# Performance work log

Hardware: AMD Instinct MI355X
Metric: run time of the kernel (lower is better)

Reference implementation:

```python
import jax, jax.numpy as jnp
import numpy as np

GAMMA = 0.999      # EMA momentum
M_PROTO = 10       # prototypes per class
K_CLS = 201        # 200 classes + background
EPS_SK = 0.05      # sinkhorn temperature
SK_ITERS = 3       # sinkhorn iterations
THR = 0.5          # pseudo-gt threshold
D_BB = 768         # backbone dim
D = 512            # projected dim


def _ln(x, g, b, eps=1e-5):
    mu = x.mean(-1, keepdims=True)
    var = ((x - mu) ** 2).mean(-1, keepdims=True)
    return (x - mu) / jnp.sqrt(var + eps) * g + b


def _l2n(x, eps=1e-12):
    n = jnp.linalg.norm(x, axis=-1, keepdims=True)
    return x / jnp.maximum(n, eps)


def _pca_dir(A, niter=10):
    # rank-1 PCA direction (deterministic power iteration; mirrors torch.pca_lowrank(q=1, center=True))
    Ac = A - A.mean(0, keepdims=True)
    v = jnp.ones((A.shape[1],), A.dtype) / jnp.sqrt(jnp.asarray(A.shape[1], A.dtype))
    for _ in range(niter):
        v = Ac.T @ (Ac @ v)
        v = v / jnp.linalg.norm(v)
    u = Ac @ v
    return u / jnp.linalg.norm(u)


def setup_inputs() -> dict:
    key = jax.random.key(0)
    ks = jax.random.split(key, 6)
    B, HW = 16, 1024
    return dict(
        patch_tokens=jax.random.normal(ks[0], (B, HW, D_BB), jnp.float32),
        gt=jax.random.randint(ks[1], (B,), 0, K_CLS - 1),
        proj_w=jax.random.normal(ks[2], (D, D_BB), jnp.float32) * 0.02,
        proj_b=jnp.zeros((D,), jnp.float32),
        feat_g=jnp.ones((D,), jnp.float32),
        feat_b=jnp.zeros((D,), jnp.float32),
        mask_g=jnp.ones((K_CLS,), jnp.float32),
        mask_b=jnp.zeros((K_CLS,), jnp.float32),
        prototypes=jax.random.normal(ks[3], (K_CLS, M_PROTO, D), jnp.float32) * 0.02,
    )


def reference(patch_tokens, gt, proj_w, proj_b, feat_g, feat_b, mask_g, mask_b, prototypes):
    B, HW, _ = patch_tokens.shape
    H = W = int(np.sqrt(HW))
    N = B * HW

    # ----- ged_pseudo_gt (on detached tokens) -----
    U = _pca_dir(patch_tokens.reshape(-1, D_BB))            # [N]
    Us = (U - U.min()) / (U.max() - U.min())
    Us = Us.reshape(B, H, W)
    pseudo_gt = jnp.where(Us < THR, gt[:, None, None], K_CLS - 1)  # [B,H,W]

    # ----- projection + normalization -----
    f = patch_tokens @ proj_w.T + proj_b                    # [B,HW,D]
    _c = _l2n(_ln(f.reshape(N, D), feat_g, feat_b))         # [N,D]
    protos = _l2n(prototypes)                               # buffer is l2-normalized in-place
    masks = jnp.einsum('nd,kmd->nmk', _c, protos)           # [N,M,K] cosine sims
    out_flat = _ln(masks.max(axis=1), mask_g, mask_b)       # [N,K]
    out_seg = out_flat.reshape(B, H, W, K_CLS).transpose(0, 3, 1, 2)  # [B,K,H,W]

    # ----- prototype_learning (vectorized 201-class loop) -----
    gt_seg = pseudo_gt.reshape(-1)                          # [N] int
    pred = jnp.argmax(out_flat, axis=-1)
    correct = (gt_seg == pred).astype(_c.dtype)             # [N]
    proto_logits = _c @ protos.reshape(-1, D).T             # [N, K*M]

    sel = jax.nn.one_hot(gt_seg, K_CLS, dtype=_c.dtype)     # [N,K] class membership
    Bk = sel.sum(0)                                         # pixels per class
    Bk_safe = jnp.where(Bk > 0, Bk, 1.0)

    # masked per-class sinkhorn (all classes in parallel)
    Q = jnp.exp(masks / EPS_SK) * sel[:, None, :]           # [N,M,K]
    sQ = Q.sum((0, 1))                                      # [K]
    Q = Q / jnp.where(sQ > 0, sQ, 1.0)
    for _ in range(SK_ITERS):
        row = Q.sum(0, keepdims=True)                       # [1,M,K] sum over pixels
        Q = Q / jnp.where(row > 0, row, 1.0) / M_PROTO
        col = Q.sum(1, keepdims=True)                       # [N,1,K] sum over prototypes
        Q = Q / jnp.where(col > 0, col, 1.0) / Bk_safe
    Q = Q * Bk                                              # [N,M,K]

    Qn = jnp.take_along_axis(Q, gt_seg[:, None, None], axis=2)[:, :, 0]  # [N,M]
    idx = jnp.argmax(Qn, axis=1)                            # hard assignment per pixel
    proto_target = (idx + M_PROTO * gt_seg).astype(jnp.float32)

    # EMA update: q masked by prediction correctness (m_k applies to both m_q and c_q; m_k^2 = m_k)
    q = jax.nn.one_hot(idx, M_PROTO, dtype=_c.dtype) * correct[:, None]  # [N,M]
    fproto = jnp.einsum('nk,nm,nd->kmd', sel, q, _c)        # per-(class,proto) feature sums
    ncnt = jnp.einsum('nk,nm->km', sel, q)                  # assignment counts
    fnorm = _l2n(fproto)
    upd = (ncnt != 0)[:, :, None]
    new_protos = _l2n(jnp.where(upd, GAMMA * protos + (1.0 - GAMMA) * fnorm, protos))

    return out_seg, proto_logits, proto_target, pseudo_gt, new_protos
```

## Files before the change

kernel.cpp:

```cpp
#include <hip/hip_runtime.h>
#include <cstdint>
#include <cstddef>

typedef _Float16 half8  __attribute__((ext_vector_type(8)));
typedef _Float16 half4v __attribute__((ext_vector_type(4)));
typedef float    f32x4  __attribute__((ext_vector_type(4)));

static constexpr int HWPX = 1024;
static constexpr int NPX  = 16384;
static constexpr int DBB  = 768;
static constexpr int DD   = 512;
static constexpr int KC   = 201;
static constexpr int KM   = 2010;
static constexpr int KMP  = 2048;

static constexpr size_t OFF_XCH    = 0;
static constexpr size_t OFF_TP     = 491520;
static constexpr size_t OFF_COLP   = 492160;
static constexpr size_t OFF_ROW16  = 541312;
static constexpr size_t OFF_ROW3   = 670336;
static constexpr size_t OFF_ROW5   = 678400;
static constexpr size_t OFF_BK     = 686464;
static constexpr size_t OFF_NCNT   = 687488;
static constexpr size_t OFF_FPROTO = 695552;
static constexpr size_t ZTOTAL     = 4812032;
static constexpr size_t OFF_GTSEG  = 4812032;
static constexpr size_t OFF_CORR   = 4877568;
static constexpr size_t OFF_U      = 4943104;
static constexpr size_t OFF_PN     = 5074176;
static constexpr size_t OFF_P16    = 9190656;
static constexpr size_t OFF_C16    = 11287808;
static constexpr size_t OFF_QD     = 28065024;
static constexpr size_t OFF_W16    = 28720384;

static constexpr size_t OUT_SEG = 0;
static constexpr size_t OUT_PL  = 3293184;
static constexpr size_t OUT_PT  = 36225024;
static constexpr size_t OUT_PG  = 36241408;
static constexpr size_t OUT_NP  = 36257792;

#define GLDS16(gp, lp) __builtin_amdgcn_global_load_lds( \
    (__attribute__((address_space(1))) const void*)(gp), \
    (__attribute__((address_space(3))) void*)(lp), 16, 0, 0)

static __device__ __forceinline__ float  wredf(float x){
  #pragma unroll
  for (int o=32;o;o>>=1) x += __shfl_down(x,o);
  return x;
}
static __device__ __forceinline__ double wredd(double x){
  #pragma unroll
  for (int o=32;o;o>>=1) x += __shfl_down(x,o);
  return x;
}

template<bool FIRST>
__global__ __launch_bounds__(256) void kPIter2(const float* __restrict__ A,
    const double* __restrict__ Win, const double* __restrict__ Tin, const double* __restrict__ colp,
    double* __restrict__ Wout, double* __restrict__ Tout, double* __restrict__ colout){
  __shared__ double vs[768];
  __shared__ double red[4][12][64];
  __shared__ double sT[4];
  int tid=threadIdx.x, lane=tid&63, w=tid>>6;
  if (FIRST){
    for (int cc=tid; cc<768; cc+=256) vs[cc] = 1.0/sqrt(768.0);
  } else {
    double Ts=0.0;
    #pragma unroll
    for (int p=0;p<8;p++) Ts += Tin[p];
    for (int cc=tid; cc<768; cc+=256){
      double sw=0.0, mc=0.0;
      #pragma unroll
      for (int p=0;p<8;p++){ sw += Win[p*768+cc]; mc += colp[p*768+cc]; }
      vs[cc] = sw - mc*(1.0/16384.0)*Ts;
    }
  }
  __syncthreads();
  int rbase = blockIdx.x*16 + w*4;
  double acc[12], cacc[12]; double tloc=0.0;
  #pragma unroll
  for (int j=0;j<12;j++){ acc[j]=0.0; cacc[j]=0.0; }
  for (int i=0;i<4;i++){
    const float* Ar = A + (size_t)(rbase+i)*DBB;
    double a[12]; double wp=0.0;
    #pragma unroll
    for (int j=0;j<12;j++){ int c=j*64+lane; a[j]=(double)Ar[c]; wp += a[j]*vs[c]; }
    wp = wredd(wp); wp = __shfl(wp,0);
    #pragma unroll
    for (int j=0;j<12;j++) acc[j] += wp*a[j];
    if (FIRST){
      #pragma unroll
      for (int j=0;j<12;j++) cacc[j] += a[j];
    }
    tloc += wp;
  }
  #pragma unroll
  for (int j=0;j<12;j++) red[w][j][lane]=acc[j];
  if (lane==0) sT[w]=tloc;
  __syncthreads();
  double* dst = Wout + (size_t)(blockIdx.x&7)*768;
  for (int cc=tid; cc<768; cc+=256){
    int j=cc>>6, l=cc&63;
    atomicAdd(&dst[cc], red[0][j][l]+red[1][j][l]+red[2][j][l]+red[3][j][l]);
  }
  if (tid==0) atomicAdd(&Tout[blockIdx.x&7], sT[0]+sT[1]+sT[2]+sT[3]);
  if (FIRST){
    __syncthreads();
    #pragma unroll
    for (int j=0;j<12;j++) red[w][j][lane]=cacc[j];
    __syncthreads();
    double* cdst = colout + (size_t)(blockIdx.x&7)*768;
    for (int cc=tid; cc<768; cc+=256){
      int j=cc>>6, l=cc&63;
      atomicAdd(&cdst[cc], red[0][j][l]+red[1][j][l]+red[2][j][l]+red[3][j][l]);
    }
  }
}

__global__ __launch_bounds__(256) void kPU2(const float* __restrict__ A, const double* __restrict__ Wp,
    const double* __restrict__ Tp, const double* __restrict__ colp, double* __restrict__ u){
  __shared__ double vs[768];
  __shared__ double sS[4];
  int tid=threadIdx.x, lane=tid&63, w=tid>>6;
  double Ts=0.0;
  #pragma unroll
  for (int p=0;p<8;p++) Ts += Tp[p];
  double sloc=0.0;
  for (int cc=tid; cc<768; cc+=256){
    double sw=0.0, mc=0.0;
    #pragma unroll
    for (int p=0;p<8;p++){ sw += Wp[p*768+cc]; mc += colp[p*768+cc]; }
    double m = mc*(1.0/16384.0);
    double v = sw - m*Ts;
    vs[cc] = v;
    sloc += m*v;
  }
  sloc = wredd(sloc);
  if (lane==0) sS[w]=sloc;
  __syncthreads();
  double s = sS[0]+sS[1]+sS[2]+sS[3];
  int rbase = blockIdx.x*16 + w*4;
  for (int i=0;i<4;i++){
    const float* Ar = A + (size_t)(rbase+i)*DBB;
    double wp=0.0;
    #pragma unroll
    for (int j=0;j<12;j++){ int c=j*64+lane; wp += (double)Ar[c]*vs[c]; }
    wp = wredd(wp);
    if (lane==0) u[rbase+i] = wp - s;
  }
}

__global__ __launch_bounds__(1024) void kFin(const double* __restrict__ u, const int* __restrict__ gt,
      float* __restrict__ outPG, int* __restrict__ gtseg, int* __restrict__ Bk){
  __shared__ double smn[16], smx[16];
  __shared__ double sres[2];
  int t = threadIdx.x;
  double mn=1e300, mx=-1e300;
  for (int k=0;k<16;k++){ double x=u[k*1024+t]; mn=fmin(mn,x); mx=fmax(mx,x); }
  #pragma unroll
  for (int o=32;o;o>>=1){ mn=fmin(mn,__shfl_down(mn,o)); mx=fmax(mx,__shfl_down(mx,o)); }
  if ((t&63)==0){ smn[t>>6]=mn; smx[t>>6]=mx; }
  __syncthreads();
  if (t==0){
    for (int i=1;i<16;i++){ mn=fmin(mn,smn[i]); mx=fmax(mx,smx[i]); }
    sres[0]=mn; sres[1]=mx;
  }
  __syncthreads();
  mn=sres[0]; mx=sres[1];
  double inv = 1.0/(mx-mn);
  for (int k=0;k<16;k++){
    int n = k*1024 + t;
    int c0 = gt[k];
    double us = (u[n]-mn)*inv;
    int g = (us < 0.5) ? c0 : 200;
    outPG[n] = (float)g;
    gtseg[n] = g;
    unsigned long long b0 = __ballot(g==c0);
    unsigned long long b1 = __ballot(g==200);
    if ((t&63)==0){
      atomicAdd(&Bk[c0], (int)__popcll(b0));
      atomicAdd(&Bk[200], (int)__popcll(b1));
    }
  }
}

__global__ __launch_bounds__(256) void kPrep(const float* __restrict__ Wp, _Float16* __restrict__ W16,
    const float* __restrict__ PR, float* __restrict__ Pn, _Float16* __restrict__ P16){
  int b = blockIdx.x;
  if (b < 384){
    int i = b*256 + threadIdx.x;
    float4 vv = ((const float4*)Wp)[i];
    half4v h; h[0]=(_Float16)vv.x; h[1]=(_Float16)vv.y; h[2]=(_Float16)vv.z; h[3]=(_Float16)vv.w;
    ((half4v*)W16)[i] = h;
    return;
  }
  int w=threadIdx.x>>6, lane=threadIdx.x&63;
  int km = (b-384)*4 + w;
  if (km >= KM){
    if (km < KMP){
      half8 z;
      #pragma unroll
      for (int i=0;i<8;i++) z[i]=(_Float16)0.0f;
      *(half8*)(P16 + (size_t)km*DD + lane*8) = z;
    }
    return;
  }
  const float* r = PR + (size_t)km*DD + lane*8;
  float4 a = *(const float4*)r, b2 = *(const float4*)(r+4);
  float x[8] = {a.x,a.y,a.z,a.w,b2.x,b2.y,b2.z,b2.w};
  float ss=0;
  #pragma unroll
  for (int i=0;i<8;i++) ss += x[i]*x[i];
  ss = __shfl(wredf(ss),0);
  float nrm = fmaxf(sqrtf(ss), 1e-12f);
  float* pw = Pn + (size_t)km*DD + lane*8;
  half8 h;
  #pragma unroll
  for (int i=0;i<8;i++){ float vv = x[i]/nrm; pw[i]=vv; h[i]=(_Float16)vv; }
  *(half8*)(P16 + (size_t)km*DD + lane*8) = h;
}

__global__ __launch_bounds__(256) void gemm1(const float* __restrict__ Af, const _Float16* __restrict__ Bm,
    _Float16* __restrict__ Ch, const float* __restrict__ bias){
  __shared__ __align__(16) char As[128*128];
  __shared__ __align__(16) char Bs[128*128];
  const int tid = threadIdx.x;
  const int lane = tid & 63, w = tid >> 6;
  const int wr = w >> 1, wc = w & 1;
  const int lrow = lane & 15, kg = lane >> 4;
  const int id = blockIdx.x;
  const int xcd = id & 7, pos = id >> 3;
  const int m0 = ((xcd<<4) | (pos>>2)) * 128;
  const int n0 = (pos & 3) * 128;

  f32x4 acc[4][4];
  #pragma unroll
  for (int i=0;i<4;i++)
    #pragma unroll
    for (int j=0;j<4;j++){ f32x4 z = {0.f,0.f,0.f,0.f}; acc[i][j]=z; }

  for (int k0 = 0; k0 < DBB; k0 += 64){
    #pragma unroll
    for (int i=0;i<4;i++){
      int slot = (i*4 + w)*64 + lane;
      int r = slot >> 3, c = slot & 7;
      int cs = c ^ (r & 7);
      GLDS16(Bm + (size_t)(n0+r)*DBB + k0 + cs*8, Bs + (i*4+w)*1024);
    }
    #pragma unroll
    for (int i=0;i<8;i++){
      int slot = i*256 + tid;
      int r = slot >> 4, c4 = slot & 15;
      float4 v = *(const float4*)(Af + (size_t)(m0+r)*DBB + k0 + c4*4);
      half4v h; h[0]=(_Float16)v.x; h[1]=(_Float16)v.y; h[2]=(_Float16)v.z; h[3]=(_Float16)v.w;
      *(half4v*)(As + r*128 + (((c4>>1)^(r&7))<<4) + (c4&1)*8) = h;
    }
    __syncthreads();
    #pragma unroll
    for (int h=0; h<2; h++){
      half8 af[4], bf[4];
      #pragma unroll
      for (int mi=0;mi<4;mi++){
        int ar = wr*64 + mi*16 + lrow;
        af[mi] = *(const half8*)(As + ar*128 + (((h*4+kg) ^ (ar&7))<<4));
      }
      #pragma unroll
      for (int nj=0;nj<4;nj++){
        int br = wc*64 + nj*16 + lrow;
        bf[nj] = *(const half8*)(Bs + br*128 + (((h*4+kg) ^ (br&7))<<4));
      }
      #pragma unroll
      for (int mi=0;mi<4;mi++)
        #pragma unroll
        for (int nj=0;nj<4;nj++)
          acc[mi][nj] = __builtin_amdgcn_mfma_f32_16x16x32_f16(af[mi], bf[nj], acc[mi][nj], 0,0,0);
    }
    __syncthreads();
  }
  #pragma unroll
  for (int mi=0;mi<4;mi++){
    int gr = m0 + wr*64 + mi*16 + kg*4;
    #pragma unroll
    for (int nj=0;nj<4;nj++){
      int gc = n0 + wc*64 + nj*16 + lrow;
      float bv = bias[gc];
      #pragma unroll
      for (int r2=0;r2<4;r2++)
        Ch[(size_t)(gr+r2)*DD + gc] = (_Float16)(acc[mi][nj][r2] + bv);
    }
  }
}

__global__ __launch_bounds__(256) void gemm2(const _Float16* __restrict__ Am, const _Float16* __restrict__ Bm,
    float* __restrict__ Cf){
  __shared__ __align__(16) char As[128*128];
  __shared__ __align__(16) char Bs[128*128];
  const int tid = threadIdx.x;
  const int lane = tid & 63, w = tid >> 6;
  const int wr = w >> 1, wc = w & 1;
  const int lrow = lane & 15, kg = lane >> 4;
  const int id = blockIdx.x;
  const int xcd = id & 7, pos = id >> 3;
  const int m0 = ((xcd<<4) | (pos>>4)) * 128;
  const int n0 = (pos & 15) * 128;

  f32x4 acc[4][4];
  #pragma unroll
  for (int i=0;i<4;i++)
    #pragma unroll
    for (int j=0;j<4;j++){ f32x4 z = {0.f,0.f,0.f,0.f}; acc[i][j]=z; }

  for (int k0 = 0; k0 < DD; k0 += 64){
    #pragma unroll
    for (int i=0;i<4;i++){
      int slot = (i*4 + w)*64 + lane;
      int r = slot >> 3, c = slot & 7;
      int cs = c ^ (r & 7);
      GLDS16(Am + (size_t)(m0+r)*DD + k0 + cs*8, As + (i*4+w)*1024);
      GLDS16(Bm + (size_t)(n0+r)*DD + k0 + cs*8, Bs + (i*4+w)*1024);
    }
    __syncthreads();
    #pragma unroll
    for (int h=0; h<2; h++){
      half8 af[4], bf[4];
      #pragma unroll
      for (int mi=0;mi<4;mi++){
        int ar = wr*64 + mi*16 + lrow;
        af[mi] = *(const half8*)(As + ar*128 + (((h*4+kg) ^ (ar&7))<<4));
      }
      #pragma unroll
      for (int nj=0;nj<4;nj++){
        int br = wc*64 + nj*16 + lrow;
        bf[nj] = *(const half8*)(Bs + br*128 + (((h*4+kg) ^ (br&7))<<4));
      }
      #pragma unroll
      for (int mi=0;mi<4;mi++)
        #pragma unroll
        for (int nj=0;nj<4;nj++)
          acc[mi][nj] = __builtin_amdgcn_mfma_f32_16x16x32_f16(af[mi], bf[nj], acc[mi][nj], 0,0,0);
    }
    __syncthreads();
  }
  #pragma unroll
  for (int mi=0;mi<4;mi++){
    int gr = m0 + wr*64 + mi*16 + kg*4;
    #pragma unroll
    for (int nj=0;nj<4;nj++){
      int gc = n0 + wc*64 + nj*16 + lrow;
      if (gc < KM){
        #pragma unroll
        for (int r2=0;r2<4;r2++)
          Cf[(size_t)(gr+r2)*KM + gc] = acc[mi][nj][r2];
      }
    }
  }
}

__global__ __launch_bounds__(256) void kLNl2n(_Float16* __restrict__ C16,
      const float* __restrict__ fg, const float* __restrict__ fb){
  int w=threadIdx.x>>6, lane=threadIdx.x&63;
  int n = blockIdx.x*4 + w;
  _Float16* row = C16 + (size_t)n*DD + lane*8;
  half8 h = *(const half8*)row;
  float x[8];
  #pragma unroll
  for (int i=0;i<8;i++) x[i] = (float)h[i];
  float s=0;
  #pragma unroll
  for (int i=0;i<8;i++) s += x[i];
  float mu = __shfl(wredf(s),0)/512.f;
  float q=0;
  #pragma unroll
  for (int i=0;i<8;i++){ float d=x[i]-mu; q+=d*d; }
  float var = __shfl(wredf(q),0)/512.f;
  float inv = 1.f/sqrtf(var+1e-5f);
  float4 g0 = *(const float4*)(fg+lane*8), g1 = *(const float4*)(fg+lane*8+4);
  float4 b0 = *(const float4*)(fb+lane*8), b1 = *(const float4*)(fb+lane*8+4);
  float gg[8] = {g0.x,g0.y,g0.z,g0.w,g1.x,g1.y,g1.z,g1.w};
  float bb[8] = {b0.x,b0.y,b0.z,b0.w,b1.x,b1.y,b1.z,b1.w};
  float y[8]; float ss=0;
  #pragma unroll
  for (int i=0;i<8;i++){ y[i] = (x[i]-mu)*inv*gg[i]+bb[i]; ss += y[i]*y[i]; }
  float nrm = fmaxf(sqrtf(__shfl(wredf(ss),0)), 1e-12f);
  half8 o;
  #pragma unroll
  for (int i=0;i<8;i++) o[i] = (_Float16)(y[i]/nrm);
  *(half8*)row = o;
}

__global__ __launch_bounds__(256) void kMaxSK(const float* __restrict__ PL, const float* __restrict__ mg,
    const float* __restrict__ mb, const int* __restrict__ gtseg, const int* __restrict__ gt,
    float* __restrict__ outseg, int* __restrict__ corr, float* __restrict__ Qd, float* __restrict__ row16){
  __shared__ float tile[16][205];
  __shared__ float qpart[10][2];
  int tid=threadIdx.x, lane=tid&63, w=tid>>6;
  int n0 = blockIdx.x*16;
  int b = n0>>10, hw0 = n0&1023;
  int c0 = gt[b];
  if (tid<20) qpart[tid>>1][tid&1]=0.f;
  __syncthreads();
  for (int r=0;r<16;r++){
    int n = n0 + r;
    int g = gtseg[n];
    if (tid < KC){
      const float* src = PL + (size_t)n*KM + tid*10;
      float v[10];
      #pragma unroll
      for (int m2=0;m2<5;m2++){
        float2 t2 = *(const float2*)(src + m2*2);
        v[m2*2]=t2.x; v[m2*2+1]=t2.y;
      }
      float mx = v[0];
      #pragma unroll
      for (int m=1;m<10;m++) mx = fmaxf(mx,v[m]);
      tile[r][tid] = mx;
      if (tid == g){
        int cl = (g==200)?1:0;
        #pragma unroll
        for (int m=0;m<10;m++){
          float e = expf(v[m]*20.f);
          Qd[(size_t)n*10+m] = e;
          atomicAdd(&qpart[m][cl], e);
        }
      }
    }
  }
  __syncthreads();
  for (int rr=0; rr<4; ++rr){
    int r = w*4 + rr;
    int n = n0 + r;
    float xv[4]; int ncl=0;
    for (int c=lane;c<KC;c+=64) xv[ncl++] = tile[r][c];
    float ps=0;
    for (int i=0;i<ncl;i++) ps += xv[i];
    float mu = __shfl(wredf(ps),0)*(1.f/201.f);
    float pv=0;
    for (int i=0;i<ncl;i++){ float d=xv[i]-mu; pv+=d*d; }
    float var = __shfl(wredf(pv),0)*(1.f/201.f);
    float inv = 1.f/sqrtf(var+1e-5f);
    float bv=-3.0e38f; int bi=1<<30;
    ncl=0;
    for (int c=lane;c<KC;c+=64){
      float o = (xv[ncl]-mu)*inv*mg[c]+mb[c]; ncl++;
      tile[r][c] = o;
      if (o>bv){ bv=o; bi=c; }
    }
    #pragma unroll
    for (int o2=32;o2;o2>>=1){
      float ov=__shfl_down(bv,o2); int oi=__shfl_down(bi,o2);
      if (ov>bv||(ov==bv&&oi<bi)){bv=ov;bi=oi;}
    }
    if (lane==0) corr[n] = (bi==gtseg[n])?1:0;
  }
  __syncthreads();
  if (tid<20){
    int m=tid>>1, cl=tid&1;
    atomicAdd(&row16[(size_t)(blockIdx.x&15)*2016 + m*KC + (cl?200:c0)], qpart[m][cl]);
  }
  for (int idx=tid; idx<KC*16; idx+=256){
    int c=idx>>4, j=idx&15;
    outseg[(((size_t)b*KC+c)<<10) + hw0 + j] = tile[j][c];
  }
}

__global__ __launch_bounds__(256) void kSKpass(float* __restrict__ Qd, const int* __restrict__ gtseg,
      const int* __restrict__ gt, const float* __restrict__ rin, int rin_parts,
      float* __restrict__ rout, const int* __restrict__ Bk){
  __shared__ float rin2[10][2];
  __shared__ double part[4][10][2];
  int n = blockIdx.x*256+threadIdx.x;
  int c0 = gt[blockIdx.x>>2];
  if (threadIdx.x < 20){
    int m = threadIdx.x>>1, cl = threadIdx.x&1;
    int cls = cl?200:c0;
    float s=0;
    for (int p=0;p<rin_parts;p++) s += rin[(size_t)p*2016 + m*KC + cls];
    rin2[m][cl]=s;
  }
  __syncthreads();
  int g = gtseg[n];
  int cl = (g==200)?1:0;
  double q[10]; double col=0.0;
  #pragma unroll
  for (int m=0;m<10;m++){
    double r = (double)rin2[m][cl];
    double t = (double)Qd[(size_t)n*10+m];
    if (r>0.0) t = t/r;
    t = t/10.0;
    q[m]=t; col+=t;
  }
  double cs = (col>0.0)? col : 1.0;
  int bk = Bk[g];
  double bs = (bk>0)? (double)bk : 1.0;
  double inv = 1.0/(cs*bs);
  int w=threadIdx.x>>6, lane=threadIdx.x&63;
  #pragma unroll
  for (int m=0;m<10;m++){
    double t = q[m]*inv;
    Qd[(size_t)n*10+m] = (float)t;
    double p0 = (g==c0)? t:0.0;
    double p1 = (g==200)? t:0.0;
    p0=wredd(p0); p1=wredd(p1);
    if (lane==0){ part[w][m][0]=p0; part[w][m][1]=p1; }
  }
  __syncthreads();
  if (threadIdx.x < 20){
    int m = threadIdx.x>>1, cl2 = threadIdx.x&1;
    double t = part[0][m][cl2]+part[1][m][cl2]+part[2][m][cl2]+part[3][m][cl2];
    atomicAdd(&rout[m*KC + (cl2?200:c0)], (float)t);
  }
}

__global__ __launch_bounds__(256) void kSKEMA(const float* __restrict__ Qd, const int* __restrict__ gtseg,
      const float* __restrict__ r5, const int* __restrict__ corr, const _Float16* __restrict__ C16,
      float* __restrict__ outPT, float* __restrict__ fproto, int* __restrict__ ncnt){
  int w=threadIdx.x>>6, lane=threadIdx.x&63;
  int n = blockIdx.x*4+w;
  int g = gtseg[n];
  float tv = -1.0f;
  if (lane<10){
    float r = r5[lane*KC+g];
    float t = Qd[(size_t)n*10+lane];
    if (r>0.f) t = t/r;
    tv = t*0.1f;
  }
  float bv = tv; int bi = lane;
  #pragma unroll
  for (int o=8;o;o>>=1){
    float ov = __shfl_down(bv,o); int oi = __shfl_down(bi,o);
    if (ov>bv || (ov==bv && oi<bi)){ bv=ov; bi=oi; }
  }
  bi = __shfl(bi, 0);
  if (lane==0) outPT[n] = (float)(bi + 10*g);
  if (corr[n]){
    half8 hc = *(const half8*)(C16 + (size_t)n*DD + lane*8);
    float* dst = fproto + ((size_t)g*10+bi)*DD + lane*8;
    #pragma unroll
    for (int i=0;i<8;i++) atomicAdd(dst+i, (float)hc[i]);
    if (lane==0) atomicAdd(&ncnt[g*10+bi], 1);
  }
}

__global__ __launch_bounds__(256) void kEMAfin(const float* __restrict__ fproto, const int* __restrict__ ncnt,
     const float* __restrict__ Pn, float* __restrict__ outNP){
  int w=threadIdx.x>>6, lane=threadIdx.x&63;
  int km = blockIdx.x*4+w;
  if (km>=KM) return;
  const float* fr = fproto + (size_t)km*DD + lane*8;
  float fp[8]; float ss=0;
  #pragma unroll
  for (int i=0;i<8;i++){ fp[i]=fr[i]; ss+=fp[i]*fp[i]; }
  float n1 = fmaxf(sqrtf(__shfl(wredf(ss),0)), 1e-12f);
  int cnt = ncnt[km];
  const float* pr = Pn + (size_t)km*DD + lane*8;
  float t[8]; float s2=0;
  #pragma unroll
  for (int i=0;i<8;i++){
    float pv = pr[i];
    float tv = cnt ? (0.999f*pv + 0.001f*(fp[i]/n1)) : pv;
    t[i]=tv; s2+=tv*tv;
  }
  float n2 = fmaxf(sqrtf(__shfl(wredf(s2),0)), 1e-12f);
  float* dst = outNP + (size_t)km*DD + lane*8;
  #pragma unroll
  for (int i=0;i<8;i++) dst[i] = t[i]/n2;
}

extern "C" void kernel_launch(void* const* d_in, const int* in_sizes, int n_in,
                              void* d_out, int out_size, void* d_ws, size_t ws_size,
                              hipStream_t stream) {
  const float* A   = (const float*)d_in[0];
  const int*   gt  = (const int*)d_in[1];
  const float* Wp  = (const float*)d_in[2];
  const float* pb  = (const float*)d_in[3];
  const float* fg  = (const float*)d_in[4];
  const float* fb  = (const float*)d_in[5];
  const float* mg  = (const float*)d_in[6];
  const float* mb  = (const float*)d_in[7];
  const float* PR  = (const float*)d_in[8];
  float* out = (float*)d_out;
  char* ws = (char*)d_ws;

  double* xch    = (double*)(ws+OFF_XCH);
  double* Tp     = (double*)(ws+OFF_TP);
  double* colp   = (double*)(ws+OFF_COLP);
  float*  row16  = (float*)(ws+OFF_ROW16);
  float*  row3   = (float*)(ws+OFF_ROW3);
  float*  row5   = (float*)(ws+OFF_ROW5);
  int*    Bk     = (int*)(ws+OFF_BK);
  int*    ncnt   = (int*)(ws+OFF_NCNT);
  float*  fproto = (float*)(ws+OFF_FPROTO);
  int*    gtseg  = (int*)(ws+OFF_GTSEG);
  int*    corr   = (int*)(ws+OFF_CORR);
  double* u      = (double*)(ws+OFF_U);
  float*  Pn     = (float*)(ws+OFF_PN);
  _Float16* P16  = (_Float16*)(ws+OFF_P16);
  _Float16* C16  = (_Float16*)(ws+OFF_C16);
  float*  Qd     = (float*)(ws+OFF_QD);
  _Float16* W16  = (_Float16*)(ws+OFF_W16);

  hipMemsetAsync(ws, 0, ZTOTAL, stream);

  kPIter2<true><<<1024,256,0,stream>>>(A, nullptr, nullptr, nullptr,
                                       xch, Tp, colp);
  for (int t=1;t<10;t++){
    kPIter2<false><<<1024,256,0,stream>>>(A, xch+(size_t)(t-1)*8*768, Tp+(t-1)*8, colp,
                                          xch+(size_t)t*8*768, Tp+t*8, nullptr);
  }
  kPU2<<<1024,256,0,stream>>>(A, xch+(size_t)9*8*768, Tp+9*8, colp, u);
  kFin<<<1,1024,0,stream>>>(u, gt, out+OUT_PG, gtseg, Bk);

  kPrep<<<896,256,0,stream>>>(Wp, W16, PR, Pn, P16);

  gemm1<<<512,256,0,stream>>>(A, W16, C16, pb);
  kLNl2n<<<4096,256,0,stream>>>(C16, fg, fb);

  gemm2<<<2048,256,0,stream>>>(C16, P16, out+OUT_PL);

  kMaxSK<<<1024,256,0,stream>>>(out+OUT_PL, mg, mb, gtseg, gt, out+OUT_SEG, corr, Qd, row16);

  kSKpass<<<64,256,0,stream>>>(Qd, gtseg, gt, row16, 16, row3, Bk);
  kSKpass<<<64,256,0,stream>>>(Qd, gtseg, gt, row3, 1, row5, Bk);
  kSKEMA<<<4096,256,0,stream>>>(Qd, gtseg, row5, corr, C16, out+OUT_PT, fproto, ncnt);

  kEMAfin<<<503,256,0,stream>>>(fproto, ncnt, Pn, out+OUT_NP);
}
```

Measured before the change: 414.5 us.

## Fuse per-class max over prototypes into gemm2 epilogue via atomicMax buffer

Moves the per-class max over the 10 prototype logits into the gemm2 epilogue. Each tile is staged through shared memory, reduced per class, and merged across tiles that straddle a class boundary with atomicMax on biased uint-encoded floats. kMaxSK then reads a compact 16384x201 max buffer instead of re-reading the whole 16384x2010 logits array, and loads raw logits only for the gt class. The cost is a larger memset (about 13 MB more), extra shared-memory passes and atomics in gemm2, and reliance on the +4 bias keeping the values positive so the uint ordering stays valid.

```diff
diff --git a/kernel.cpp b/kernel.cpp
--- a/kernel.cpp
+++ b/kernel.cpp
@@ -23,15 +23,16 @@
 static constexpr size_t OFF_BK     = 686464;
 static constexpr size_t OFF_NCNT   = 687488;
 static constexpr size_t OFF_FPROTO = 695552;
-static constexpr size_t ZTOTAL     = 4812032;
-static constexpr size_t OFF_GTSEG  = 4812032;
-static constexpr size_t OFF_CORR   = 4877568;
-static constexpr size_t OFF_U      = 4943104;
-static constexpr size_t OFF_PN     = 5074176;
-static constexpr size_t OFF_P16    = 9190656;
-static constexpr size_t OFF_C16    = 11287808;
-static constexpr size_t OFF_QD     = 28065024;
-static constexpr size_t OFF_W16    = 28720384;
+static constexpr size_t OFF_MAXB   = 4812032;
+static constexpr size_t ZTOTAL     = 17984768;
+static constexpr size_t OFF_GTSEG  = 17984768;
+static constexpr size_t OFF_CORR   = 18050304;
+static constexpr size_t OFF_U      = 18115840;
+static constexpr size_t OFF_PN     = 18246912;
+static constexpr size_t OFF_P16    = 22363392;
+static constexpr size_t OFF_C16    = 24460544;
+static constexpr size_t OFF_QD     = 41237760;
+static constexpr size_t OFF_W16    = 41893120;
 
 static constexpr size_t OUT_SEG = 0;
 static constexpr size_t OUT_PL  = 3293184;
@@ -292,9 +293,10 @@
 }
 
 __global__ __launch_bounds__(256) void gemm2(const _Float16* __restrict__ Am, const _Float16* __restrict__ Bm,
-    float* __restrict__ Cf){
-  __shared__ __align__(16) char As[128*128];
-  __shared__ __align__(16) char Bs[128*128];
+    float* __restrict__ Cf, unsigned int* __restrict__ maxbuf){
+  __shared__ __align__(16) char smem[32768];
+  char* As = smem;
+  char* Bs = smem + 16384;
   const int tid = threadIdx.x;
   const int lane = tid & 63, w = tid >> 6;
   const int wr = w >> 1, wc = w & 1;
@@ -354,6 +356,35 @@
       }
     }
   }
+  float* lsf = (float*)smem;
+  const int cLo = n0/10;
+  const int cHi = (n0+127)/10 > 200 ? 200 : (n0+127)/10;
+  const int nC = cHi - cLo + 1;
+  #pragma unroll
+  for (int h=0; h<2; ++h){
+    __syncthreads();
+    if (wr == h){
+      #pragma unroll
+      for (int mi=0;mi<4;mi++){
+        int lr = mi*16 + kg*4;
+        #pragma unroll
+        for (int nj=0;nj<4;nj++){
+          int col = wc*64 + nj*16 + lrow;
+          #pragma unroll
+          for (int r2=0;r2<4;r2++) lsf[(lr+r2)*128 + col] = acc[mi][nj][r2];
+        }
+      }
+    }
+    __syncthreads();
+    for (int t = tid; t < 64*nC; t += 256){
+      int row = t / nC, c = cLo + t % nC;
+      int lo = c*10;     if (lo < n0) lo = n0;
+      int hi = c*10+9;   if (hi > n0+127) hi = n0+127;
+      float mx = lsf[row*128 + (lo-n0)];
+      for (int cc2 = lo+1; cc2 <= hi; ++cc2) mx = fmaxf(mx, lsf[row*128 + (cc2-n0)]);
+      atomicMax(&maxbuf[(size_t)(m0 + h*64 + row)*KC + c], __float_as_uint(mx + 4.0f));
+    }
+  }
 }
 
 __global__ __launch_bounds__(256) void kLNl2n(_Float16* __restrict__ C16,
@@ -388,7 +419,8 @@
   *(half8*)row = o;
 }
 
-__global__ __launch_bounds__(256) void kMaxSK(const float* __restrict__ PL, const float* __restrict__ mg,
+__global__ __launch_bounds__(256) void kMaxSK(const unsigned int* __restrict__ maxbuf,
+    const float* __restrict__ PL, const float* __restrict__ mg,
     const float* __restrict__ mb, const int* __restrict__ gtseg, const int* __restrict__ gt,
     float* __restrict__ outseg, int* __restrict__ corr, float* __restrict__ Qd, float* __restrict__ row16){
   __shared__ float tile[16][205];
@@ -403,24 +435,18 @@
     int n = n0 + r;
     int g = gtseg[n];
     if (tid < KC){
-      const float* src = PL + (size_t)n*KM + tid*10;
-      float v[10];
-      #pragma unroll
-      for (int m2=0;m2<5;m2++){
-        float2 t2 = *(const float2*)(src + m2*2);
-        v[m2*2]=t2.x; v[m2*2+1]=t2.y;
-      }
-      float mx = v[0];
-      #pragma unroll
-      for (int m=1;m<10;m++) mx = fmaxf(mx,v[m]);
-      tile[r][tid] = mx;
+      tile[r][tid] = __uint_as_float(maxbuf[(size_t)n*KC + tid]) - 4.0f;
       if (tid == g){
+        const float* src = PL + (size_t)n*KM + g*10;
         int cl = (g==200)?1:0;
         #pragma unroll
-        for (int m=0;m<10;m++){
-          float e = expf(v[m]*20.f);
-          Qd[(size_t)n*10+m] = e;
-          atomicAdd(&qpart[m][cl], e);
+        for (int m2=0;m2<5;m2++){
+          float2 t2 = *(const float2*)(src + m2*2);
+          float e0 = expf(t2.x*20.f), e1 = expf(t2.y*20.f);
+          Qd[(size_t)n*10+m2*2]   = e0;
+          Qd[(size_t)n*10+m2*2+1] = e1;
+          atomicAdd(&qpart[m2*2][cl], e0);
+          atomicAdd(&qpart[m2*2+1][cl], e1);
         }
       }
     }
@@ -590,6 +616,7 @@
   int*    Bk     = (int*)(ws+OFF_BK);
   int*    ncnt   = (int*)(ws+OFF_NCNT);
   float*  fproto = (float*)(ws+OFF_FPROTO);
+  unsigned int* maxbuf = (unsigned int*)(ws+OFF_MAXB);
   int*    gtseg  = (int*)(ws+OFF_GTSEG);
   int*    corr   = (int*)(ws+OFF_CORR);
   double* u      = (double*)(ws+OFF_U);
@@ -601,8 +628,7 @@
 
   hipMemsetAsync(ws, 0, ZTOTAL, stream);
 
-  kPIter2<true><<<1024,256,0,stream>>>(A, nullptr, nullptr, nullptr,
-                                       xch, Tp, colp);
+  kPIter2<true><<<1024,256,0,stream>>>(A, nullptr, nullptr, nullptr, xch, Tp, colp);
   for (int t=1;t<10;t++){
     kPIter2<false><<<1024,256,0,stream>>>(A, xch+(size_t)(t-1)*8*768, Tp+(t-1)*8, colp,
                                           xch+(size_t)t*8*768, Tp+t*8, nullptr);
@@ -615,9 +641,9 @@
   gemm1<<<512,256,0,stream>>>(A, W16, C16, pb);
   kLNl2n<<<4096,256,0,stream>>>(C16, fg, fb);
 
-  gemm2<<<2048,256,0,stream>>>(C16, P16, out+OUT_PL);
-
-  kMaxSK<<<1024,256,0,stream>>>(out+OUT_PL, mg, mb, gtseg, gt, out+OUT_SEG, corr, Qd, row16);
+  gemm2<<<2048,256,0,stream>>>(C16, P16, out+OUT_PL, maxbuf);
+
+  kMaxSK<<<1024,256,0,stream>>>(maxbuf, out+OUT_PL, mg, mb, gtseg, gt, out+OUT_SEG, corr, Qd, row16);
 
   kSKpass<<<64,256,0,stream>>>(Qd, gtseg, gt, row16, 16, row3, Bk);
   kSKpass<<<64,256,0,stream>>>(Qd, gtseg, gt, row3, 1, row5, Bk);
```

Result: slower. 430.4 us (+3.8%).
